# Kernel optimization log

Hardware: AMD Instinct MI355X
Metric: run time of the kernel (lower is better)

Reference implementation:

```python
import jax, jax.numpy as jnp
import numpy as np

B, S, D, H = 2, 2048, 1024, 16
DK = D // H
FF_HIDDEN = 2048  # FeedForward default hidden_dim (fixed, not 4*D)


def setup_inputs() -> dict:
    key = jax.random.key(0)
    ks = jax.random.split(key, 16)
    s = 0.02
    inp = {
        "query": jax.random.normal(ks[0], (B, S, D), jnp.float32),
        "key": jax.random.normal(ks[1], (B, S, D), jnp.float32),
        "value": jax.random.normal(ks[2], (B, S, D), jnp.float32),
        "Wq": jax.random.normal(ks[3], (D, D), jnp.float32) * s,
        "bq": jnp.zeros((D,), jnp.float32),
        "Wk": jax.random.normal(ks[4], (D, D), jnp.float32) * s,
        "bk": jnp.zeros((D,), jnp.float32),
        "Wv": jax.random.normal(ks[5], (D, D), jnp.float32) * s,
        "bv": jnp.zeros((D,), jnp.float32),
        "ln_g": jnp.ones((D,), jnp.float32),
        "ln_b": jnp.zeros((D,), jnp.float32),
        "W1": jax.random.normal(ks[6], (D, FF_HIDDEN), jnp.float32) * s,
        "b1": jnp.zeros((FF_HIDDEN,), jnp.float32),
        "W2": jax.random.normal(ks[7], (FF_HIDDEN, D), jnp.float32) * s,
        "b2": jnp.zeros((D,), jnp.float32),
    }
    return inp


def reference(query, key, value, Wq, bq, Wk, bk, Wv, bv, ln_g, ln_b, W1, b1, W2, b2):
    # QKV projections
    q = query @ Wq + bq  # [B,S,D]
    k = key @ Wk + bk
    v = value @ Wv + bv
    # split heads -> [B,H,S,DK]
    q = q.reshape(B, S, H, DK).transpose(0, 2, 1, 3)
    k = k.reshape(B, S, H, DK).transpose(0, 2, 1, 3)
    v = v.reshape(B, S, H, DK).transpose(0, 2, 1, 3)
    # naive attention: full [B,H,S,S] scores (faithful to source)
    scores = jnp.einsum("bhqd,bhkd->bhqk", q, k) / jnp.sqrt(jnp.float32(DK))
    probs = jax.nn.softmax(scores, axis=-1)  # dropout = identity (eval)
    attn = jnp.einsum("bhqk,bhkd->bhqd", probs, v)
    attn = attn.transpose(0, 2, 1, 3).reshape(B, S, D)
    # LayerNorm
    mu = attn.mean(axis=-1, keepdims=True)
    var = attn.var(axis=-1, keepdims=True)
    ffi = (attn - mu) / jnp.sqrt(var + 1e-5) * ln_g + ln_b
    # FeedForward (dropout = identity in eval)
    h = jax.nn.relu(ffi @ W1 + b1)
    ff = h @ W2 + b2
    return ffi + ff
```

## Files before the change

### kernel.cpp

```cpp
#include <hip/hip_runtime.h>
#include <hip/hip_bf16.h>


#define S_LEN 2048
#define DMODEL 1024
#define NROWS 4096
#define QSCALE (0.125f * 1.4426950408889634f)

typedef __attribute__((ext_vector_type(8))) short short8_t;
typedef __attribute__((ext_vector_type(4))) float f32x4;

__device__ __forceinline__ unsigned short f2bf(float f){
  union { float f; unsigned int u; } a; a.f = f;
  unsigned int r = a.u + 0x7fffu + ((a.u >> 16) & 1u);
  return (unsigned short)(r >> 16);
}
__device__ __forceinline__ unsigned int pack2(float lo, float hi){
  return (unsigned int)f2bf(lo) | ((unsigned int)f2bf(hi) << 16);
}
__device__ __forceinline__ unsigned int cvtpk(float lo, float hi){
  unsigned int r;
  asm("v_cvt_pk_bf16_f32 %0, %1, %2" : "=v"(r) : "v"(lo), "v"(hi));
  return r;
}
__device__ __forceinline__ void gload_lds16(const void* g, void* l){
  __builtin_amdgcn_global_load_lds((const __attribute__((address_space(1))) unsigned int*)g,
                                   (__attribute__((address_space(3))) unsigned int*)l, 16, 0, 0);
}

__global__ __launch_bounds__(256) void cast3_kernel(const float* __restrict__ q,
    const float* __restrict__ k, const float* __restrict__ v, unsigned short* __restrict__ out){
  const float* src = blockIdx.y == 0 ? q : (blockIdx.y == 1 ? k : v);
  size_t i = (size_t)(blockIdx.x * 256 + threadIdx.x) * 8;
  float4 a = *(const float4*)(src + i);
  float4 b = *(const float4*)(src + i + 4);
  uint4 u; u.x = pack2(a.x,a.y); u.y = pack2(a.z,a.w); u.z = pack2(b.x,b.y); u.w = pack2(b.z,b.w);
  *(uint4*)(out + (size_t)blockIdx.y*4194304 + i) = u;
}

__device__ __forceinline__ void tc_body(const float* __restrict__ in,
    unsigned short* __restrict__ out, int R, int C, int bx, int by){
  __shared__ __align__(16) unsigned short tile[64*76];
  int c0 = bx * 64, r0 = by * 64;
  int t = threadIdx.x;
#pragma unroll
  for (int i = 0; i < 4; i++){
    int slot = i*256 + t;
    int r = slot >> 4, c4 = slot & 15;
    float4 v = *(const float4*)(in + (size_t)(r0 + r)*C + c0 + c4*4);
    ushort4 u; u.x = f2bf(v.x); u.y = f2bf(v.y); u.z = f2bf(v.z); u.w = f2bf(v.w);
    *(ushort4*)&tile[r*76 + c4*4] = u;
  }
  __syncthreads();
#pragma unroll
  for (int i = 0; i < 4; i++){
    int slot = i*256 + t;
    int oc = slot >> 4, seg = slot & 15;
    ushort4 u;
    u.x = tile[(seg*4+0)*76 + oc];
    u.y = tile[(seg*4+1)*76 + oc];
    u.z = tile[(seg*4+2)*76 + oc];
    u.w = tile[(seg*4+3)*76 + oc];
    *(ushort4*)(out + (size_t)(c0 + oc)*R + r0 + seg*4) = u;
  }
}
__global__ __launch_bounds__(256) void transpose_cast_f32(const float* __restrict__ in,
    unsigned short* __restrict__ out, int R, int C){
  tc_body(in, out, R, C, blockIdx.x, blockIdx.y);
}
__global__ __launch_bounds__(256) void transpose_cast_w3(const float* __restrict__ w0,
    const float* __restrict__ w1, const float* __restrict__ w2, unsigned short* __restrict__ out){
  const float* in = blockIdx.z == 0 ? w0 : (blockIdx.z == 1 ? w1 : w2);
  tc_body(in, out + (size_t)blockIdx.z*1048576, 1024, 1024, blockIdx.x, blockIdx.y);
}

__global__ __launch_bounds__(256) void transpose_bf16(const unsigned short* __restrict__ in,
    unsigned short* __restrict__ out, int R, int C, int inStride){
  __shared__ __align__(16) unsigned short tile[64*76];
  int c0 = blockIdx.x * 64, r0 = blockIdx.y * 64;
  int t = threadIdx.x;
#pragma unroll
  for (int i = 0; i < 2; i++){
    int slot = i*256 + t;
    int r = slot >> 3, c8 = slot & 7;
    uint4 v = *(const uint4*)(in + (size_t)(r0 + r)*inStride + c0 + c8*8);
    uint2 lo; lo.x = v.x; lo.y = v.y;
    uint2 hi; hi.x = v.z; hi.y = v.w;
    *(uint2*)&tile[r*76 + c8*8]     = lo;
    *(uint2*)&tile[r*76 + c8*8 + 4] = hi;
  }
  __syncthreads();
#pragma unroll
  for (int i = 0; i < 4; i++){
    int slot = i*256 + t;
    int oc = slot >> 4, seg = slot & 15;
    ushort4 u;
    u.x = tile[(seg*4+0)*76 + oc];
    u.y = tile[(seg*4+1)*76 + oc];
    u.z = tile[(seg*4+2)*76 + oc];
    u.w = tile[(seg*4+3)*76 + oc];
    *(ushort4*)(out + (size_t)(c0 + oc)*R + r0 + seg*4) = u;
  }
}

__global__ __launch_bounds__(256) void concat_bias(const float* __restrict__ a,
    const float* __restrict__ b, const float* __restrict__ c, float* __restrict__ o){
  int i = blockIdx.x*256 + threadIdx.x;
  o[i] = i < 1024 ? a[i] : (i < 2048 ? b[i-1024] : c[i-2048]);
}

template<bool OBF16, bool RELU, bool RESID, int NF>
__global__ __launch_bounds__(256, 2) void gemm_bt(
    const unsigned short* __restrict__ A, const unsigned short* __restrict__ Bt,
    const float* __restrict__ bias, float scale, int scale_ncols, size_t aSel,
    unsigned short* __restrict__ Ob, float* __restrict__ Of,
    const float* __restrict__ resid, int M, int N, int K)
{
  __shared__ __align__(16) unsigned short As[2*128*64];
  __shared__ __align__(16) unsigned short Bs[2*32*NF*64];
  char* AsB = (char*)As;
  char* BsB = (char*)Bs;
  int tid = threadIdx.x, lane = tid & 63, wave = tid >> 6;
  int wr = wave >> 1, wc = wave & 1;
  int m0 = blockIdx.y * 128, n0 = blockIdx.x * (32*NF);
  int qr = lane & 15, g = lane >> 4;
  f32x4 acc[4][NF];
#pragma unroll
  for (int i = 0; i < 4; i++)
#pragma unroll
    for (int j = 0; j < NF; j++) acc[i][j] = (f32x4){0.f,0.f,0.f,0.f};

  int lr = lane >> 3, ls = lane & 7;
  int scol = (ls ^ lr) * 8;
  const unsigned short* Ag = A + (size_t)(n0 >> 10)*aSel + (size_t)(m0 + wave*32 + lr)*K + scol;
  const unsigned short* Bg = Bt + (size_t)(n0 + wave*8*NF + lr)*K + scol;

  int rx = qr & 7;
  int aoff = (wr*64 + qr)*128 + ((g ^ rx) << 4);
  int boff = (wc*16*NF + qr)*128 + ((g ^ rx) << 4);

  int NT = K >> 6;
#pragma unroll
  for (int i = 0; i < 4; i++)
    gload_lds16(Ag + (size_t)i*8*K, AsB + wave*4096 + i*1024);
#pragma unroll
  for (int i = 0; i < NF; i++)
    gload_lds16(Bg + (size_t)i*8*K, BsB + wave*NF*1024 + i*1024);

  for (int it = 0; it < NT; ++it){
    int cur = it & 1;
    if (it + 1 < NT){
      int k1 = (it + 1) << 6;
      char* ad = AsB + (cur^1)*16384 + wave*4096;
      char* bd = BsB + (cur^1)*NF*4096 + wave*NF*1024;
#pragma unroll
      for (int i = 0; i < 4; i++)
        gload_lds16(Ag + (size_t)i*8*K + k1, ad + i*1024);
#pragma unroll
      for (int i = 0; i < NF; i++)
        gload_lds16(Bg + (size_t)i*8*K + k1, bd + i*1024);
      if constexpr (NF == 4) asm volatile("s_waitcnt vmcnt(8)" ::: "memory");
      else                   asm volatile("s_waitcnt vmcnt(6)" ::: "memory");
    } else {
      asm volatile("s_waitcnt vmcnt(0)" ::: "memory");
    }
    __builtin_amdgcn_s_barrier();
    asm volatile("" ::: "memory");

    const char* ka = AsB + cur*16384;
    const char* kb = BsB + cur*NF*4096;
    short8_t af[2][4], bfv[2][NF];
#pragma unroll
    for (int mi = 0; mi < 4; mi++){
      af[0][mi] = *(const short8_t*)(ka + aoff + mi*2048);
      af[1][mi] = *(const short8_t*)(ka + (aoff^64) + mi*2048);
    }
#pragma unroll
    for (int ni = 0; ni < NF; ni++){
      bfv[0][ni] = *(const short8_t*)(kb + boff + ni*2048);
      bfv[1][ni] = *(const short8_t*)(kb + (boff^64) + ni*2048);
    }
#pragma unroll
    for (int kh = 0; kh < 2; kh++)
#pragma unroll
      for (int mi = 0; mi < 4; mi++)
#pragma unroll
        for (int ni = 0; ni < NF; ni++)
          acc[mi][ni] = __builtin_amdgcn_mfma_f32_16x16x32_bf16(af[kh][mi], bfv[kh][ni], acc[mi][ni], 0, 0, 0);

    asm volatile("s_waitcnt lgkmcnt(0)" ::: "memory");
    __builtin_amdgcn_s_barrier();
    asm volatile("" ::: "memory");
  }
#pragma unroll
  for (int ni = 0; ni < NF; ni++){
    int col = n0 + wc*16*NF + ni*16 + qr;
    float bs = bias[col];
    float sc = (col < scale_ncols) ? scale : 1.f;
#pragma unroll
    for (int mi = 0; mi < 4; mi++){
#pragma unroll
      for (int r = 0; r < 4; r++){
        int row = m0 + wr*64 + mi*16 + g*4 + r;
        float v = (acc[mi][ni][r] + bs) * sc;
        if constexpr (RELU) v = fmaxf(v, 0.f);
        if constexpr (RESID) v += resid[(size_t)row*N + col];
        if constexpr (OBF16) Ob[(size_t)row*N + col] = f2bf(v);
        else                 Of[(size_t)row*N + col] = v;
      }
    }
  }
}

__global__ __launch_bounds__(256, 2) void flash_attn(
    const unsigned short* __restrict__ qkv,
    const unsigned short* __restrict__ vT,
    float* __restrict__ attn)
{
  __shared__ __align__(16) char smem[49152];
  int tid = threadIdx.x, lane = tid & 63, wave = tid >> 6;
  int bid = blockIdx.x;
  int orig = (bid & 7) * 64 + (bid >> 3);
  int bh = orig >> 4, qb = orig & 15;
  int b = bh >> 4, hd = bh & 15;
  int q0 = qb * 128 + wave * 32;
  int qr = lane & 15, g = lane >> 4;

  short8_t qf[2][2];
#pragma unroll
  for (int qg = 0; qg < 2; qg++){
    const unsigned short* qptr = qkv + (size_t)(b*S_LEN + q0 + 16*qg + qr)*3072 + hd*64 + g*8;
    qf[qg][0] = *(const short8_t*)qptr;
    qf[qg][1] = *(const short8_t*)(qptr + 32);
  }

  const f32x4 z4 = {0.f,0.f,0.f,0.f};
  f32x4 oacc[4][2];
#pragma unroll
  for (int tv = 0; tv < 4; tv++)
#pragma unroll
    for (int qg = 0; qg < 2; qg++) oacc[tv][qg] = z4;
  float lsum[2] = {0.f, 0.f};

  int lrow = lane >> 3, lslot = lane & 7;
  int sw = (lslot ^ lrow) * 8;
  const unsigned short* kg = qkv + 1024 + (size_t)(b*S_LEN + wave*8 + lrow)*3072 + hd*64 + sw;
  const unsigned short* vg = vT + (size_t)(hd*64 + wave*8 + lrow)*4096 + b*S_LEN + sw;

  int rx = qr & 7;
  int koff0 = qr*128 + ((g ^ rx) * 16);
  int koff1 = koff0 ^ 64;

  char* Pb = smem + 32768 + wave*4096;
  int gh = g >> 1;
  int pw0 = qr*128 + 8*(g & 1);
  int pr0 = qr*128;

  {
    char* kb_ = smem + wave*1024;
    char* vb_ = smem + 16384 + wave*1024;
    gload_lds16(kg,                       kb_);
    gload_lds16(kg + (size_t)32*3072,     kb_ + 4096);
    gload_lds16(vg,                       vb_);
    gload_lds16(vg + (size_t)32*4096,     vb_ + 4096);
  }

  int cur = 0;
  for (int it = 0; it < S_LEN/64; ++it){
    if (it + 1 < S_LEN/64){
      int kv1 = (it + 1) * 64;
      char* kb_ = smem + (cur^1)*8192 + wave*1024;
      char* vb_ = smem + 16384 + (cur^1)*8192 + wave*1024;
      gload_lds16(kg + (size_t)kv1*3072,        kb_);
      gload_lds16(kg + (size_t)(kv1+32)*3072,   kb_ + 4096);
      gload_lds16(vg + kv1,                     vb_);
      gload_lds16(vg + (size_t)32*4096 + kv1,   vb_ + 4096);
      asm volatile("s_waitcnt vmcnt(4)" ::: "memory");
    } else {
      asm volatile("s_waitcnt vmcnt(0)" ::: "memory");
    }
    __builtin_amdgcn_s_barrier();
    asm volatile("" ::: "memory");

    const char* kb = smem + cur*8192;
    const char* vb = smem + 16384 + cur*8192;

    f32x4 st[4][2];
    __builtin_amdgcn_s_setprio(1);
#pragma unroll
    for (int t = 0; t < 4; t++){
      short8_t kf0 = *(const short8_t*)(kb + koff0 + t*2048);
      short8_t kf1 = *(const short8_t*)(kb + koff1 + t*2048);
#pragma unroll
      for (int qg = 0; qg < 2; qg++){
        st[t][qg] = __builtin_amdgcn_mfma_f32_16x16x32_bf16(kf0, qf[qg][0], z4, 0, 0, 0);
        st[t][qg] = __builtin_amdgcn_mfma_f32_16x16x32_bf16(kf1, qf[qg][1], st[t][qg], 0, 0, 0);
      }
    }
    __builtin_amdgcn_s_setprio(0);

#pragma unroll
    for (int qg = 0; qg < 2; qg++){
      float ps0 = 0.f, ps1 = 0.f;
#pragma unroll
      for (int t = 0; t < 4; t++){
        float p0 = exp2f(st[t][qg][0]);
        float p1 = exp2f(st[t][qg][1]);
        float p2 = exp2f(st[t][qg][2]);
        float p3 = exp2f(st[t][qg][3]);
        uint2 wv; wv.x = cvtpk(p0, p1); wv.y = cvtpk(p2, p3);
        *(uint2*)(Pb + qg*2048 + pw0 + (((2*t + gh) ^ rx) << 4)) = wv;
        ps0 += p0 + p1;
        ps1 += p2 + p3;
      }
      lsum[qg] += ps0 + ps1;
    }

    short8_t pf[2][2];
#pragma unroll
    for (int qg = 0; qg < 2; qg++){
      pf[0][qg] = *(const short8_t*)(Pb + qg*2048 + pr0 + (((0 + g) ^ rx) << 4));
      pf[1][qg] = *(const short8_t*)(Pb + qg*2048 + pr0 + (((4 + g) ^ rx) << 4));
    }

    __builtin_amdgcn_s_setprio(1);
#pragma unroll
    for (int tv = 0; tv < 4; tv++){
      short8_t vf0 = *(const short8_t*)(vb + koff0 + tv*2048);
      short8_t vf1 = *(const short8_t*)(vb + koff1 + tv*2048);
#pragma unroll
      for (int qg = 0; qg < 2; qg++){
        oacc[tv][qg] = __builtin_amdgcn_mfma_f32_16x16x32_bf16(vf0, pf[0][qg], oacc[tv][qg], 0, 0, 0);
        oacc[tv][qg] = __builtin_amdgcn_mfma_f32_16x16x32_bf16(vf1, pf[1][qg], oacc[tv][qg], 0, 0, 0);
      }
    }
    __builtin_amdgcn_s_setprio(0);

    asm volatile("s_waitcnt lgkmcnt(0)" ::: "memory");
    __builtin_amdgcn_s_barrier();
    asm volatile("" ::: "memory");
    cur ^= 1;
  }
  float inv[2];
#pragma unroll
  for (int qg = 0; qg < 2; qg++){
    float l = lsum[qg];
    l += __shfl_xor(l, 16, 64);
    l += __shfl_xor(l, 32, 64);
    inv[qg] = 1.f / l;
  }

  __syncthreads();
  float* ot = (float*)(smem + wave*8320);
#pragma unroll
  for (int qg = 0; qg < 2; qg++)
#pragma unroll
    for (int tv = 0; tv < 4; tv++)
#pragma unroll
      for (int r = 0; r < 4; r++)
        ot[(qg*16 + qr)*65 + tv*16 + g*4 + r] = oacc[tv][qg][r] * inv[qg];
  __syncthreads();
  int seg = lane & 3;
#pragma unroll
  for (int rr = 0; rr < 2; rr++){
    int row = rr*16 + (lane >> 2);
    const float* src = ot + row*65 + seg*16;
    float* dst = attn + (size_t)(b*S_LEN + qb*128 + wave*32 + row)*DMODEL + hd*64 + seg*16;
#pragma unroll
    for (int i = 0; i < 4; i++){
      float4 v; v.x = src[i*4]; v.y = src[i*4+1]; v.z = src[i*4+2]; v.w = src[i*4+3];
      *(float4*)(dst + i*4) = v;
    }
  }
}

__global__ __launch_bounds__(256) void layernorm_kernel(const float* __restrict__ x,
    const float* __restrict__ gw, const float* __restrict__ bw,
    float* __restrict__ y, unsigned short* __restrict__ yb)
{
  int row = blockIdx.x, t = threadIdx.x;
  float4 v = *(const float4*)(x + (size_t)row*DMODEL + t*4);
  float s = (v.x + v.y) + (v.z + v.w);
  float q = (v.x*v.x + v.y*v.y) + (v.z*v.z + v.w*v.w);
#pragma unroll
  for (int off = 1; off < 64; off <<= 1){
    s += __shfl_xor(s, off, 64);
    q += __shfl_xor(q, off, 64);
  }
  __shared__ float red[8];
  if ((t & 63) == 0){ red[(t >> 6)*2] = s; red[(t >> 6)*2 + 1] = q; }
  __syncthreads();
  s = red[0] + red[2] + red[4] + red[6];
  q = red[1] + red[3] + red[5] + red[7];
  float mu = s * (1.f/DMODEL);
  float var = q * (1.f/DMODEL) - mu*mu;
  float rstd = rsqrtf(var + 1e-5f);
  float4 gg = *(const float4*)(gw + t*4);
  float4 bb = *(const float4*)(bw + t*4);
  float4 o;
  o.x = (v.x - mu)*rstd*gg.x + bb.x;
  o.y = (v.y - mu)*rstd*gg.y + bb.y;
  o.z = (v.z - mu)*rstd*gg.z + bb.z;
  o.w = (v.w - mu)*rstd*gg.w + bb.w;
  *(float4*)(y + (size_t)row*DMODEL + t*4) = o;
  uint2 u; u.x = pack2(o.x, o.y); u.y = pack2(o.z, o.w);
  *(uint2*)(yb + (size_t)row*DMODEL + t*4) = u;
}

extern "C" void kernel_launch(void* const* d_in, const int* in_sizes, int n_in,
                              void* d_out, int out_size, void* d_ws, size_t ws_size,
                              hipStream_t stream)
{
  const float* query = (const float*)d_in[0];
  const float* key_  = (const float*)d_in[1];
  const float* value = (const float*)d_in[2];
  const float* Wq = (const float*)d_in[3];
  const float* bq = (const float*)d_in[4];
  const float* Wk = (const float*)d_in[5];
  const float* bk = (const float*)d_in[6];
  const float* Wv = (const float*)d_in[7];
  const float* bv = (const float*)d_in[8];
  const float* ln_g = (const float*)d_in[9];
  const float* ln_b = (const float*)d_in[10];
  const float* W1 = (const float*)d_in[11];
  const float* b1 = (const float*)d_in[12];
  const float* W2 = (const float*)d_in[13];
  const float* b2 = (const float*)d_in[14];

  char* ws = (char*)d_ws;
  unsigned short* qx     = (unsigned short*)(ws + 0);
  unsigned short* WqkvT  = (unsigned short*)(ws + 25165824);
  unsigned short* W1T    = (unsigned short*)(ws + 31457280);
  unsigned short* W2T    = (unsigned short*)(ws + 35651584);
  unsigned short* qkvbuf = (unsigned short*)(ws + 39845888);
  unsigned short* vTb    = (unsigned short*)(ws + 65011712);
  float*          attnf  = (float*)(ws + 73400320);
  unsigned short* hbuf   = (unsigned short*)(ws + 73400320);
  float*          biascat= (float*)(ws + 73400320 + 8388608);
  float*          ffif   = (float*)(ws + 90177536);
  unsigned short* ffib   = (unsigned short*)(ws + 106954752);

  cast3_kernel<<<dim3(2048,3), 256, 0, stream>>>(query, key_, value, qx);
  transpose_cast_w3<<<dim3(16,16,3), 256, 0, stream>>>(Wq, Wk, Wv, WqkvT);
  transpose_cast_f32<<<dim3(32,16), 256, 0, stream>>>(W1, W1T, 1024, 2048);
  transpose_cast_f32<<<dim3(16,32), 256, 0, stream>>>(W2, W2T, 2048, 1024);
  concat_bias<<<12, 256, 0, stream>>>(bq, bk, bv, biascat);

  gemm_bt<true,false,false,4><<<dim3(24,32), 256, 0, stream>>>(
      qx, WqkvT, biascat, QSCALE, 1024, (size_t)4194304, qkvbuf, nullptr, nullptr, 4096, 3072, 1024);
  transpose_bf16<<<dim3(16,64), 256, 0, stream>>>(qkvbuf + 2048, vTb, 4096, 1024, 3072);
  flash_attn<<<512, 256, 0, stream>>>(qkvbuf, vTb, attnf);
  layernorm_kernel<<<4096, 256, 0, stream>>>(attnf, ln_g, ln_b, ffif, ffib);
  gemm_bt<true,true,false,4><<<dim3(16,32), 256, 0, stream>>>(
      ffib, W1T, b1, 1.f, 0, (size_t)0, hbuf, nullptr, nullptr, 4096, 2048, 1024);
  gemm_bt<false,false,true,2><<<dim3(16,32), 256, 0, stream>>>(
      hbuf, W2T, b2, 1.f, 0, (size_t)0, nullptr, (float*)d_out, ffif, 4096, 1024, 2048);
}
```

Measured before the change: 197.8 us.

## Fuse input cast and V transpose into QKV GEMM, use bf16 residual

The QKV GEMM now loads f32 activations directly, converts them to bf16 in registers and stores them to LDS, which removes the separate cast kernel and its intermediate buffer. Its epilogue writes the V section already transposed, which removes the transpose kernel. LayerNorm no longer writes an f32 copy, and the final GEMM reads the bf16 LayerNorm output as its residual. This saves kernel launches and global memory traffic. In exchange, the QKV A-load path is register-staged with synchronous barriers, and the residual carries bf16 rounding.

```diff
diff --git a/kernel.cpp b/kernel.cpp
--- a/kernel.cpp
+++ b/kernel.cpp
@@ -18,6 +18,10 @@
 __device__ __forceinline__ unsigned int pack2(float lo, float hi){
   return (unsigned int)f2bf(lo) | ((unsigned int)f2bf(hi) << 16);
 }
+__device__ __forceinline__ float bf2f(unsigned short u){
+  union { unsigned int u; float f; } a; a.u = ((unsigned int)u) << 16;
+  return a.f;
+}
 __device__ __forceinline__ unsigned int cvtpk(float lo, float hi){
   unsigned int r;
   asm("v_cvt_pk_bf16_f32 %0, %1, %2" : "=v"(r) : "v"(lo), "v"(hi));
@@ -26,16 +30,6 @@
 __device__ __forceinline__ void gload_lds16(const void* g, void* l){
   __builtin_amdgcn_global_load_lds((const __attribute__((address_space(1))) unsigned int*)g,
                                    (__attribute__((address_space(3))) unsigned int*)l, 16, 0, 0);
-}
-
-__global__ __launch_bounds__(256) void cast3_kernel(const float* __restrict__ q,
-    const float* __restrict__ k, const float* __restrict__ v, unsigned short* __restrict__ out){
-  const float* src = blockIdx.y == 0 ? q : (blockIdx.y == 1 ? k : v);
-  size_t i = (size_t)(blockIdx.x * 256 + threadIdx.x) * 8;
-  float4 a = *(const float4*)(src + i);
-  float4 b = *(const float4*)(src + i + 4);
-  uint4 u; u.x = pack2(a.x,a.y); u.y = pack2(a.z,a.w); u.z = pack2(b.x,b.y); u.w = pack2(b.z,b.w);
-  *(uint4*)(out + (size_t)blockIdx.y*4194304 + i) = u;
 }
 
 __device__ __forceinline__ void tc_body(const float* __restrict__ in,
@@ -74,47 +68,21 @@
   tc_body(in, out + (size_t)blockIdx.z*1048576, 1024, 1024, blockIdx.x, blockIdx.y);
 }
 
-__global__ __launch_bounds__(256) void transpose_bf16(const unsigned short* __restrict__ in,
-    unsigned short* __restrict__ out, int R, int C, int inStride){
-  __shared__ __align__(16) unsigned short tile[64*76];
-  int c0 = blockIdx.x * 64, r0 = blockIdx.y * 64;
-  int t = threadIdx.x;
-#pragma unroll
-  for (int i = 0; i < 2; i++){
-    int slot = i*256 + t;
-    int r = slot >> 3, c8 = slot & 7;
-    uint4 v = *(const uint4*)(in + (size_t)(r0 + r)*inStride + c0 + c8*8);
-    uint2 lo; lo.x = v.x; lo.y = v.y;
-    uint2 hi; hi.x = v.z; hi.y = v.w;
-    *(uint2*)&tile[r*76 + c8*8]     = lo;
-    *(uint2*)&tile[r*76 + c8*8 + 4] = hi;
-  }
-  __syncthreads();
-#pragma unroll
-  for (int i = 0; i < 4; i++){
-    int slot = i*256 + t;
-    int oc = slot >> 4, seg = slot & 15;
-    ushort4 u;
-    u.x = tile[(seg*4+0)*76 + oc];
-    u.y = tile[(seg*4+1)*76 + oc];
-    u.z = tile[(seg*4+2)*76 + oc];
-    u.w = tile[(seg*4+3)*76 + oc];
-    *(ushort4*)(out + (size_t)(c0 + oc)*R + r0 + seg*4) = u;
-  }
-}
-
 __global__ __launch_bounds__(256) void concat_bias(const float* __restrict__ a,
     const float* __restrict__ b, const float* __restrict__ c, float* __restrict__ o){
   int i = blockIdx.x*256 + threadIdx.x;
   o[i] = i < 1024 ? a[i] : (i < 2048 ? b[i-1024] : c[i-2048]);
 }
 
-template<bool OBF16, bool RELU, bool RESID, int NF>
+template<bool OBF16, bool RELU, bool RESID, int NF, bool AF32, bool WV>
 __global__ __launch_bounds__(256, 2) void gemm_bt(
-    const unsigned short* __restrict__ A, const unsigned short* __restrict__ Bt,
-    const float* __restrict__ bias, float scale, int scale_ncols, size_t aSel,
+    const void* __restrict__ Av, const float* __restrict__ Aq,
+    const float* __restrict__ Ak, const float* __restrict__ Avv,
+    const unsigned short* __restrict__ Bt,
+    const float* __restrict__ bias, float scale, int scale_ncols,
     unsigned short* __restrict__ Ob, float* __restrict__ Of,
-    const float* __restrict__ resid, int M, int N, int K)
+    const unsigned short* __restrict__ resid, unsigned short* __restrict__ vtOut,
+    int M, int N, int K)
 {
   __shared__ __align__(16) unsigned short As[2*128*64];
   __shared__ __align__(16) unsigned short Bs[2*32*NF*64];
@@ -132,7 +100,6 @@
 
   int lr = lane >> 3, ls = lane & 7;
   int scol = (ls ^ lr) * 8;
-  const unsigned short* Ag = A + (size_t)(n0 >> 10)*aSel + (size_t)(m0 + wave*32 + lr)*K + scol;
   const unsigned short* Bg = Bt + (size_t)(n0 + wave*8*NF + lr)*K + scol;
 
   int rx = qr & 7;
@@ -140,58 +107,133 @@
   int boff = (wc*16*NF + qr)*128 + ((g ^ rx) << 4);
 
   int NT = K >> 6;
-#pragma unroll
-  for (int i = 0; i < 4; i++)
-    gload_lds16(Ag + (size_t)i*8*K, AsB + wave*4096 + i*1024);
-#pragma unroll
-  for (int i = 0; i < NF; i++)
-    gload_lds16(Bg + (size_t)i*8*K, BsB + wave*NF*1024 + i*1024);
-
-  for (int it = 0; it < NT; ++it){
-    int cur = it & 1;
-    if (it + 1 < NT){
-      int k1 = (it + 1) << 6;
-      char* ad = AsB + (cur^1)*16384 + wave*4096;
-      char* bd = BsB + (cur^1)*NF*4096 + wave*NF*1024;
-#pragma unroll
-      for (int i = 0; i < 4; i++)
-        gload_lds16(Ag + (size_t)i*8*K + k1, ad + i*1024);
+
+  if constexpr (AF32){
+    const float* Af = (n0 >> 10) == 0 ? Aq : ((n0 >> 10) == 1 ? Ak : Avv);
+    const float* Ag = Af + (size_t)(m0 + wave*32 + lr)*K + scol;
+    int awrite = wave*4096 + lane*16;
+
+    {
+      float4 a0[4], a1[4];
+#pragma unroll
+      for (int i = 0; i < 4; i++){
+        a0[i] = *(const float4*)(Ag + (size_t)i*8*K);
+        a1[i] = *(const float4*)(Ag + (size_t)i*8*K + 4);
+      }
 #pragma unroll
       for (int i = 0; i < NF; i++)
-        gload_lds16(Bg + (size_t)i*8*K + k1, bd + i*1024);
-      if constexpr (NF == 4) asm volatile("s_waitcnt vmcnt(8)" ::: "memory");
-      else                   asm volatile("s_waitcnt vmcnt(6)" ::: "memory");
-    } else {
-      asm volatile("s_waitcnt vmcnt(0)" ::: "memory");
-    }
-    __builtin_amdgcn_s_barrier();
-    asm volatile("" ::: "memory");
-
-    const char* ka = AsB + cur*16384;
-    const char* kb = BsB + cur*NF*4096;
-    short8_t af[2][4], bfv[2][NF];
-#pragma unroll
-    for (int mi = 0; mi < 4; mi++){
-      af[0][mi] = *(const short8_t*)(ka + aoff + mi*2048);
-      af[1][mi] = *(const short8_t*)(ka + (aoff^64) + mi*2048);
-    }
-#pragma unroll
-    for (int ni = 0; ni < NF; ni++){
-      bfv[0][ni] = *(const short8_t*)(kb + boff + ni*2048);
-      bfv[1][ni] = *(const short8_t*)(kb + (boff^64) + ni*2048);
-    }
-#pragma unroll
-    for (int kh = 0; kh < 2; kh++)
-#pragma unroll
-      for (int mi = 0; mi < 4; mi++)
-#pragma unroll
-        for (int ni = 0; ni < NF; ni++)
-          acc[mi][ni] = __builtin_amdgcn_mfma_f32_16x16x32_bf16(af[kh][mi], bfv[kh][ni], acc[mi][ni], 0, 0, 0);
-
-    asm volatile("s_waitcnt lgkmcnt(0)" ::: "memory");
-    __builtin_amdgcn_s_barrier();
-    asm volatile("" ::: "memory");
-  }
+        gload_lds16(Bg + (size_t)i*8*K, BsB + wave*NF*1024 + i*1024);
+#pragma unroll
+      for (int i = 0; i < 4; i++){
+        uint4 u;
+        u.x = cvtpk(a0[i].x, a0[i].y); u.y = cvtpk(a0[i].z, a0[i].w);
+        u.z = cvtpk(a1[i].x, a1[i].y); u.w = cvtpk(a1[i].z, a1[i].w);
+        *(uint4*)(AsB + awrite + i*1024) = u;
+      }
+      __syncthreads();
+    }
+    for (int it = 0; it < NT; ++it){
+      int cur = it & 1;
+      float4 a0[4], a1[4];
+      if (it + 1 < NT){
+        int k1 = (it + 1) << 6;
+#pragma unroll
+        for (int i = 0; i < NF; i++)
+          gload_lds16(Bg + (size_t)i*8*K + k1, BsB + (cur^1)*NF*4096 + wave*NF*1024 + i*1024);
+#pragma unroll
+        for (int i = 0; i < 4; i++){
+          a0[i] = *(const float4*)(Ag + (size_t)i*8*K + k1);
+          a1[i] = *(const float4*)(Ag + (size_t)i*8*K + k1 + 4);
+        }
+      }
+      const char* ka = AsB + cur*16384;
+      const char* kb = BsB + cur*NF*4096;
+      short8_t af[2][4], bfv[2][NF];
+#pragma unroll
+      for (int mi = 0; mi < 4; mi++){
+        af[0][mi] = *(const short8_t*)(ka + aoff + mi*2048);
+        af[1][mi] = *(const short8_t*)(ka + (aoff^64) + mi*2048);
+      }
+#pragma unroll
+      for (int ni = 0; ni < NF; ni++){
+        bfv[0][ni] = *(const short8_t*)(kb + boff + ni*2048);
+        bfv[1][ni] = *(const short8_t*)(kb + (boff^64) + ni*2048);
+      }
+#pragma unroll
+      for (int kh = 0; kh < 2; kh++)
+#pragma unroll
+        for (int mi = 0; mi < 4; mi++)
+#pragma unroll
+          for (int ni = 0; ni < NF; ni++)
+            acc[mi][ni] = __builtin_amdgcn_mfma_f32_16x16x32_bf16(af[kh][mi], bfv[kh][ni], acc[mi][ni], 0, 0, 0);
+      if (it + 1 < NT){
+#pragma unroll
+        for (int i = 0; i < 4; i++){
+          uint4 u;
+          u.x = cvtpk(a0[i].x, a0[i].y); u.y = cvtpk(a0[i].z, a0[i].w);
+          u.z = cvtpk(a1[i].x, a1[i].y); u.w = cvtpk(a1[i].z, a1[i].w);
+          *(uint4*)(AsB + (cur^1)*16384 + awrite + i*1024) = u;
+        }
+      }
+      __syncthreads();
+    }
+  } else {
+    const unsigned short* Ag = (const unsigned short*)Av + (size_t)(m0 + wave*32 + lr)*K + scol;
+#pragma unroll
+    for (int i = 0; i < 4; i++)
+      gload_lds16(Ag + (size_t)i*8*K, AsB + wave*4096 + i*1024);
+#pragma unroll
+    for (int i = 0; i < NF; i++)
+      gload_lds16(Bg + (size_t)i*8*K, BsB + wave*NF*1024 + i*1024);
+
+    for (int it = 0; it < NT; ++it){
+      int cur = it & 1;
+      if (it + 1 < NT){
+        int k1 = (it + 1) << 6;
+        char* ad = AsB + (cur^1)*16384 + wave*4096;
+        char* bd = BsB + (cur^1)*NF*4096 + wave*NF*1024;
+#pragma unroll
+        for (int i = 0; i < 4; i++)
+          gload_lds16(Ag + (size_t)i*8*K + k1, ad + i*1024);
+#pragma unroll
+        for (int i = 0; i < NF; i++)
+          gload_lds16(Bg + (size_t)i*8*K + k1, bd + i*1024);
+        if constexpr (NF == 4) asm volatile("s_waitcnt vmcnt(8)" ::: "memory");
+        else                   asm volatile("s_waitcnt vmcnt(6)" ::: "memory");
+      } else {
+        asm volatile("s_waitcnt vmcnt(0)" ::: "memory");
+      }
+      __builtin_amdgcn_s_barrier();
+      asm volatile("" ::: "memory");
+
+      const char* ka = AsB + cur*16384;
+      const char* kb = BsB + cur*NF*4096;
+      short8_t af[2][4], bfv[2][NF];
+#pragma unroll
+      for (int mi = 0; mi < 4; mi++){
+        af[0][mi] = *(const short8_t*)(ka + aoff + mi*2048);
+        af[1][mi] = *(const short8_t*)(ka + (aoff^64) + mi*2048);
+      }
+#pragma unroll
+      for (int ni = 0; ni < NF; ni++){
+        bfv[0][ni] = *(const short8_t*)(kb + boff + ni*2048);
+        bfv[1][ni] = *(const short8_t*)(kb + (boff^64) + ni*2048);
+      }
+#pragma unroll
+      for (int kh = 0; kh < 2; kh++)
+#pragma unroll
+        for (int mi = 0; mi < 4; mi++)
+#pragma unroll
+          for (int ni = 0; ni < NF; ni++)
+            acc[mi][ni] = __builtin_amdgcn_mfma_f32_16x16x32_bf16(af[kh][mi], bfv[kh][ni], acc[mi][ni], 0, 0, 0);
+
+      asm volatile("s_waitcnt lgkmcnt(0)" ::: "memory");
+      __builtin_amdgcn_s_barrier();
+      asm volatile("" ::: "memory");
+    }
+  }
+
+  bool vblock = WV && (n0 >= 2048);
 #pragma unroll
   for (int ni = 0; ni < NF; ni++){
     int col = n0 + wc*16*NF + ni*16 + qr;
@@ -199,14 +241,23 @@
     float sc = (col < scale_ncols) ? scale : 1.f;
 #pragma unroll
     for (int mi = 0; mi < 4; mi++){
-#pragma unroll
-      for (int r = 0; r < 4; r++){
-        int row = m0 + wr*64 + mi*16 + g*4 + r;
-        float v = (acc[mi][ni][r] + bs) * sc;
-        if constexpr (RELU) v = fmaxf(v, 0.f);
-        if constexpr (RESID) v += resid[(size_t)row*N + col];
-        if constexpr (OBF16) Ob[(size_t)row*N + col] = f2bf(v);
-        else                 Of[(size_t)row*N + col] = v;
+      int rowb = m0 + wr*64 + mi*16 + g*4;
+      if (vblock){
+        ushort4 uv;
+        float v0 = acc[mi][ni][0] + bs, v1 = acc[mi][ni][1] + bs;
+        float v2 = acc[mi][ni][2] + bs, v3 = acc[mi][ni][3] + bs;
+        uv.x = f2bf(v0); uv.y = f2bf(v1); uv.z = f2bf(v2); uv.w = f2bf(v3);
+        *(ushort4*)(vtOut + (size_t)(col - 2048)*4096 + rowb) = uv;
+      } else {
+#pragma unroll
+        for (int r = 0; r < 4; r++){
+          int row = rowb + r;
+          float v = (acc[mi][ni][r] + bs) * sc;
+          if constexpr (RELU) v = fmaxf(v, 0.f);
+          if constexpr (RESID) v += bf2f(resid[(size_t)row*N + col]);
+          if constexpr (OBF16) Ob[(size_t)row*N + col] = f2bf(v);
+          else                 Of[(size_t)row*N + col] = v;
+        }
       }
     }
   }
@@ -376,7 +427,7 @@
 
 __global__ __launch_bounds__(256) void layernorm_kernel(const float* __restrict__ x,
     const float* __restrict__ gw, const float* __restrict__ bw,
-    float* __restrict__ y, unsigned short* __restrict__ yb)
+    unsigned short* __restrict__ yb)
 {
   int row = blockIdx.x, t = threadIdx.x;
   float4 v = *(const float4*)(x + (size_t)row*DMODEL + t*4);
@@ -402,7 +453,6 @@
   o.y = (v.y - mu)*rstd*gg.y + bb.y;
   o.z = (v.z - mu)*rstd*gg.z + bb.z;
   o.w = (v.w - mu)*rstd*gg.w + bb.w;
-  *(float4*)(y + (size_t)row*DMODEL + t*4) = o;
   uint2 u; u.x = pack2(o.x, o.y); u.y = pack2(o.z, o.w);
   *(uint2*)(yb + (size_t)row*DMODEL + t*4) = u;
 }
@@ -428,7 +478,6 @@
   const float* b2 = (const float*)d_in[14];
 
   char* ws = (char*)d_ws;
-  unsigned short* qx     = (unsigned short*)(ws + 0);
   unsigned short* WqkvT  = (unsigned short*)(ws + 25165824);
   unsigned short* W1T    = (unsigned short*)(ws + 31457280);
   unsigned short* W2T    = (unsigned short*)(ws + 35651584);
@@ -437,22 +486,22 @@
   float*          attnf  = (float*)(ws + 73400320);
   unsigned short* hbuf   = (unsigned short*)(ws + 73400320);
   float*          biascat= (float*)(ws + 73400320 + 8388608);
-  float*          ffif   = (float*)(ws + 90177536);
   unsigned short* ffib   = (unsigned short*)(ws + 106954752);
 
-  cast3_kernel<<<dim3(2048,3), 256, 0, stream>>>(query, key_, value, qx);
   transpose_cast_w3<<<dim3(16,16,3), 256, 0, stream>>>(Wq, Wk, Wv, WqkvT);
   transpose_cast_f32<<<dim3(32,16), 256, 0, stream>>>(W1, W1T, 1024, 2048);
   transpose_cast_f32<<<dim3(16,32), 256, 0, stream>>>(W2, W2T, 2048, 1024);
   concat_bias<<<12, 256, 0, stream>>>(bq, bk, bv, biascat);
 
-  gemm_bt<true,false,false,4><<<dim3(24,32), 256, 0, stream>>>(
-      qx, WqkvT, biascat, QSCALE, 1024, (size_t)4194304, qkvbuf, nullptr, nullptr, 4096, 3072, 1024);
-  transpose_bf16<<<dim3(16,64), 256, 0, stream>>>(qkvbuf + 2048, vTb, 4096, 1024, 3072);
+  gemm_bt<true,false,false,4,true,true><<<dim3(24,32), 256, 0, stream>>>(
+      nullptr, query, key_, value, WqkvT, biascat, QSCALE, 1024,
+      qkvbuf, nullptr, nullptr, vTb, 4096, 3072, 1024);
   flash_attn<<<512, 256, 0, stream>>>(qkvbuf, vTb, attnf);
-  layernorm_kernel<<<4096, 256, 0, stream>>>(attnf, ln_g, ln_b, ffif, ffib);
-  gemm_bt<true,true,false,4><<<dim3(16,32), 256, 0, stream>>>(
-      ffib, W1T, b1, 1.f, 0, (size_t)0, hbuf, nullptr, nullptr, 4096, 2048, 1024);
-  gemm_bt<false,false,true,2><<<dim3(16,32), 256, 0, stream>>>(
-      hbuf, W2T, b2, 1.f, 0, (size_t)0, nullptr, (float*)d_out, ffif, 4096, 1024, 2048);
-}
+  layernorm_kernel<<<4096, 256, 0, stream>>>(attnf, ln_g, ln_b, ffib);
+  gemm_bt<true,true,false,4,false,false><<<dim3(16,32), 256, 0, stream>>>(
+      ffib, nullptr, nullptr, nullptr, W1T, b1, 1.f, 0,
+      hbuf, nullptr, nullptr, nullptr, 4096, 2048, 1024);
+  gemm_bt<false,false,true,2,false,false><<<dim3(16,32), 256, 0, stream>>>(
+      hbuf, nullptr, nullptr, nullptr, W2T, b2, 1.f, 0,
+      nullptr, (float*)d_out, ffib, nullptr, 4096, 1024, 2048);
+}
```

After: 206.8 us. +4.5%, slower.

## Fuse V transpose into QKV GEMM epilogue and use bf16 residual

Applied to the files above, without the earlier changes.

The QKV GEMM epilogue now writes V blocks directly in transposed bf16 layout, so the separate transpose kernel and its extra read and write of V are gone. LayerNorm no longer writes an fp32 copy of its output. The final GEMM instead reads the bf16 LayerNorm output as the residual, cutting memory traffic. The cost is lower residual precision, since ffi is now added in bf16-rounded form, plus strided 8-byte stores in the V epilogue.

```diff
diff --git a/kernel.cpp b/kernel.cpp
--- a/kernel.cpp
+++ b/kernel.cpp
@@ -17,6 +17,10 @@
 }
 __device__ __forceinline__ unsigned int pack2(float lo, float hi){
   return (unsigned int)f2bf(lo) | ((unsigned int)f2bf(hi) << 16);
+}
+__device__ __forceinline__ float bf2f(unsigned short u){
+  union { unsigned int u; float f; } a; a.u = ((unsigned int)u) << 16;
+  return a.f;
 }
 __device__ __forceinline__ unsigned int cvtpk(float lo, float hi){
   unsigned int r;
@@ -74,47 +78,19 @@
   tc_body(in, out + (size_t)blockIdx.z*1048576, 1024, 1024, blockIdx.x, blockIdx.y);
 }
 
-__global__ __launch_bounds__(256) void transpose_bf16(const unsigned short* __restrict__ in,
-    unsigned short* __restrict__ out, int R, int C, int inStride){
-  __shared__ __align__(16) unsigned short tile[64*76];
-  int c0 = blockIdx.x * 64, r0 = blockIdx.y * 64;
-  int t = threadIdx.x;
-#pragma unroll
-  for (int i = 0; i < 2; i++){
-    int slot = i*256 + t;
-    int r = slot >> 3, c8 = slot & 7;
-    uint4 v = *(const uint4*)(in + (size_t)(r0 + r)*inStride + c0 + c8*8);
-    uint2 lo; lo.x = v.x; lo.y = v.y;
-    uint2 hi; hi.x = v.z; hi.y = v.w;
-    *(uint2*)&tile[r*76 + c8*8]     = lo;
-    *(uint2*)&tile[r*76 + c8*8 + 4] = hi;
-  }
-  __syncthreads();
-#pragma unroll
-  for (int i = 0; i < 4; i++){
-    int slot = i*256 + t;
-    int oc = slot >> 4, seg = slot & 15;
-    ushort4 u;
-    u.x = tile[(seg*4+0)*76 + oc];
-    u.y = tile[(seg*4+1)*76 + oc];
-    u.z = tile[(seg*4+2)*76 + oc];
-    u.w = tile[(seg*4+3)*76 + oc];
-    *(ushort4*)(out + (size_t)(c0 + oc)*R + r0 + seg*4) = u;
-  }
-}
-
 __global__ __launch_bounds__(256) void concat_bias(const float* __restrict__ a,
     const float* __restrict__ b, const float* __restrict__ c, float* __restrict__ o){
   int i = blockIdx.x*256 + threadIdx.x;
   o[i] = i < 1024 ? a[i] : (i < 2048 ? b[i-1024] : c[i-2048]);
 }
 
-template<bool OBF16, bool RELU, bool RESID, int NF>
+template<bool OBF16, bool RELU, bool RESID, int NF, bool WV>
 __global__ __launch_bounds__(256, 2) void gemm_bt(
     const unsigned short* __restrict__ A, const unsigned short* __restrict__ Bt,
     const float* __restrict__ bias, float scale, int scale_ncols, size_t aSel,
     unsigned short* __restrict__ Ob, float* __restrict__ Of,
-    const float* __restrict__ resid, int M, int N, int K)
+    const unsigned short* __restrict__ resid, unsigned short* __restrict__ vtOut,
+    int M, int N, int K)
 {
   __shared__ __align__(16) unsigned short As[2*128*64];
   __shared__ __align__(16) unsigned short Bs[2*32*NF*64];
@@ -192,6 +168,8 @@
     __builtin_amdgcn_s_barrier();
     asm volatile("" ::: "memory");
   }
+
+  bool vblock = WV && (n0 >= 2048);
 #pragma unroll
   for (int ni = 0; ni < NF; ni++){
     int col = n0 + wc*16*NF + ni*16 + qr;
@@ -199,14 +177,24 @@
     float sc = (col < scale_ncols) ? scale : 1.f;
 #pragma unroll
     for (int mi = 0; mi < 4; mi++){
-#pragma unroll
-      for (int r = 0; r < 4; r++){
-        int row = m0 + wr*64 + mi*16 + g*4 + r;
-        float v = (acc[mi][ni][r] + bs) * sc;
-        if constexpr (RELU) v = fmaxf(v, 0.f);
-        if constexpr (RESID) v += resid[(size_t)row*N + col];
-        if constexpr (OBF16) Ob[(size_t)row*N + col] = f2bf(v);
-        else                 Of[(size_t)row*N + col] = v;
+      int rowb = m0 + wr*64 + mi*16 + g*4;
+      if (vblock){
+        ushort4 uv;
+        uv.x = f2bf(acc[mi][ni][0] + bs);
+        uv.y = f2bf(acc[mi][ni][1] + bs);
+        uv.z = f2bf(acc[mi][ni][2] + bs);
+        uv.w = f2bf(acc[mi][ni][3] + bs);
+        *(ushort4*)(vtOut + (size_t)(col - 2048)*4096 + rowb) = uv;
+      } else {
+#pragma unroll
+        for (int r = 0; r < 4; r++){
+          int row = rowb + r;
+          float v = (acc[mi][ni][r] + bs) * sc;
+          if constexpr (RELU) v = fmaxf(v, 0.f);
+          if constexpr (RESID) v += bf2f(resid[(size_t)row*N + col]);
+          if constexpr (OBF16) Ob[(size_t)row*N + col] = f2bf(v);
+          else                 Of[(size_t)row*N + col] = v;
+        }
       }
     }
   }
@@ -376,7 +364,7 @@
 
 __global__ __launch_bounds__(256) void layernorm_kernel(const float* __restrict__ x,
     const float* __restrict__ gw, const float* __restrict__ bw,
-    float* __restrict__ y, unsigned short* __restrict__ yb)
+    unsigned short* __restrict__ yb)
 {
   int row = blockIdx.x, t = threadIdx.x;
   float4 v = *(const float4*)(x + (size_t)row*DMODEL + t*4);
@@ -402,7 +390,6 @@
   o.y = (v.y - mu)*rstd*gg.y + bb.y;
   o.z = (v.z - mu)*rstd*gg.z + bb.z;
   o.w = (v.w - mu)*rstd*gg.w + bb.w;
-  *(float4*)(y + (size_t)row*DMODEL + t*4) = o;
   uint2 u; u.x = pack2(o.x, o.y); u.y = pack2(o.z, o.w);
   *(uint2*)(yb + (size_t)row*DMODEL + t*4) = u;
 }
@@ -437,7 +424,6 @@
   float*          attnf  = (float*)(ws + 73400320);
   unsigned short* hbuf   = (unsigned short*)(ws + 73400320);
   float*          biascat= (float*)(ws + 73400320 + 8388608);
-  float*          ffif   = (float*)(ws + 90177536);
   unsigned short* ffib   = (unsigned short*)(ws + 106954752);
 
   cast3_kernel<<<dim3(2048,3), 256, 0, stream>>>(query, key_, value, qx);
@@ -446,13 +432,15 @@
   transpose_cast_f32<<<dim3(16,32), 256, 0, stream>>>(W2, W2T, 2048, 1024);
   concat_bias<<<12, 256, 0, stream>>>(bq, bk, bv, biascat);
 
-  gemm_bt<true,false,false,4><<<dim3(24,32), 256, 0, stream>>>(
-      qx, WqkvT, biascat, QSCALE, 1024, (size_t)4194304, qkvbuf, nullptr, nullptr, 4096, 3072, 1024);
-  transpose_bf16<<<dim3(16,64), 256, 0, stream>>>(qkvbuf + 2048, vTb, 4096, 1024, 3072);
+  gemm_bt<true,false,false,4,true><<<dim3(24,32), 256, 0, stream>>>(
+      qx, WqkvT, biascat, QSCALE, 1024, (size_t)4194304,
+      qkvbuf, nullptr, nullptr, vTb, 4096, 3072, 1024);
   flash_attn<<<512, 256, 0, stream>>>(qkvbuf, vTb, attnf);
-  layernorm_kernel<<<4096, 256, 0, stream>>>(attnf, ln_g, ln_b, ffif, ffib);
-  gemm_bt<true,true,false,4><<<dim3(16,32), 256, 0, stream>>>(
-      ffib, W1T, b1, 1.f, 0, (size_t)0, hbuf, nullptr, nullptr, 4096, 2048, 1024);
-  gemm_bt<false,false,true,2><<<dim3(16,32), 256, 0, stream>>>(
-      hbuf, W2T, b2, 1.f, 0, (size_t)0, nullptr, (float*)d_out, ffif, 4096, 1024, 2048);
-}
+  layernorm_kernel<<<4096, 256, 0, stream>>>(attnf, ln_g, ln_b, ffib);
+  gemm_bt<true,true,false,4,false><<<dim3(16,32), 256, 0, stream>>>(
+      ffib, W1T, b1, 1.f, 0, (size_t)0,
+      hbuf, nullptr, nullptr, nullptr, 4096, 2048, 1024);
+  gemm_bt<false,false,true,2,false><<<dim3(16,32), 256, 0, stream>>>(
+      hbuf, W2T, b2, 1.f, 0, (size_t)0,
+      nullptr, (float*)d_out, ffib, nullptr, 4096, 1024, 2048);
+}
```

Measured after the change: 194.1 us. Within noise of the previous version (-1.9%).
